# Performance work log

Measured on AMD Instinct MI355X. Metric: run time of the kernel, lower is better.

## Reference

```python
import jax, jax.numpy as jnp
import numpy as np
from jax import lax

IN_C, OUT_C, K, Z_DIM, GROUPS = 256, 256, 3, 64, 1
B, H, W = 16, 32, 32


def setup_inputs() -> dict:
    key = jax.random.key(0)
    k1, k2, k3 = jax.random.split(key, 3)
    x = jax.random.normal(k1, (B, IN_C, H, W), dtype=jnp.float32)
    z = jax.random.normal(k2, (B, Z_DIM), dtype=jnp.float32)
    # nn.Linear(z_dim, groups*out_per_group*in_per_group*k*k, bias=False).weight
    fan = GROUPS * (OUT_C // GROUPS) * (IN_C // GROUPS) * K * K  # 589824
    w_lin = jax.random.normal(k3, (fan, Z_DIM), dtype=jnp.float32) * (1.0 / np.sqrt(Z_DIM))
    return {"x": x, "z": z, "w_lin": w_lin}


def reference(x, z, w_lin):
    b = x.shape[0]
    in_per_group = IN_C // GROUPS
    # hypernetwork: per-sample conv weights [B, out_c, in_c/groups, k, k]
    Wgen = (z @ w_lin.T).reshape(b, OUT_C, in_per_group, K, K)
    pad = K // 2

    def conv_one(xi, Wi):
        # xi: [in_c, H, W], Wi: [out_c, in_c/groups, k, k]
        y = lax.conv_general_dilated(
            xi[None], Wi,
            window_strides=(1, 1),
            padding=[(pad, pad), (pad, pad)],
            dimension_numbers=("NCHW", "OIHW", "NCHW"),
            feature_group_count=GROUPS,
        )
        return y[0]

    return jax.vmap(conv_one)(x, Wgen)  # [B, out_c, H, W]
```

## Files before the change

### kernel.cpp

```cpp
#include <hip/hip_runtime.h>

#define PB_ 589824
#define XT_PB 295936
#define XGR 544

typedef __bf16 bf16;
typedef __bf16 bf16x4 __attribute__((ext_vector_type(4)));
typedef __bf16 bf16x8 __attribute__((ext_vector_type(8)));
typedef float f32x4 __attribute__((ext_vector_type(4)));

static __device__ inline bf16x8 cvt8(float4 a, float4 b) {
  bf16x8 r;
  r[0] = (bf16)a.x; r[1] = (bf16)a.y; r[2] = (bf16)a.z; r[3] = (bf16)a.w;
  r[4] = (bf16)b.x; r[5] = (bf16)b.y; r[6] = (bf16)b.z; r[7] = (bf16)b.w;
  return r;
}

__global__ __launch_bounds__(256) void prep_kernel(const float* __restrict__ z,
                                                   const float* __restrict__ wl,
                                                   const float* __restrict__ x,
                                                   bf16* __restrict__ WgA,
                                                   bf16* __restrict__ xt) {
  const int bid = blockIdx.x;
  if (bid < 1152) {
    __shared__ __align__(16) char wsm[16384];
    const int c_  = bid & 7;
    const int tap = (bid >> 3) % 9;
    const int ob  = bid / 72;
    const int lane = threadIdx.x & 63;
    const int wave = threadIdx.x >> 6;
    const int l15 = lane & 15;
    const int q = lane >> 4;

    const float* zp = z + l15 * 64 + q * 8;
    bf16x8 bz[2];
#pragma unroll
    for (int kc = 0; kc < 2; ++kc)
      bz[kc] = cvt8(*(const float4*)(zp + kc * 32), *(const float4*)(zp + kc * 32 + 4));

#pragma unroll
    for (int mi = 0; mi < 4; ++mi) {
      const int m = wave * 4 + mi;
#pragma unroll
      for (int h = 0; h < 2; ++h) {
        const long t = (long)(ob * 16 + m) * 2304 + (c_ * 32 + h * 16 + l15) * 9 + tap;
        const float* wp = wl + t * 64 + q * 8;
        f32x4 acc = {0.f, 0.f, 0.f, 0.f};
#pragma unroll
        for (int kc = 0; kc < 2; ++kc) {
          bf16x8 aw = cvt8(*(const float4*)(wp + kc * 32), *(const float4*)(wp + kc * 32 + 4));
          acc = __builtin_amdgcn_mfma_f32_16x16x32_bf16(aw, bz[kc], acc, 0, 0, 0);
        }
        bf16x4 o;
        o[0] = (bf16)acc[0]; o[1] = (bf16)acc[1]; o[2] = (bf16)acc[2]; o[3] = (bf16)acc[3];
        const int elem = ((h * 2 + (q >> 1)) * 16 + m) * 8 + (q & 1) * 4;
        int byte = (l15 << 10) + elem * 2;
        byte ^= (l15 & 7) << 4;
        *(bf16x4*)(wsm + byte) = o;
      }
    }
    __syncthreads();
    const int b = threadIdx.x >> 4;
    const int l16 = threadIdx.x & 15;
    const long gbase = ((((long)b * 16 + ob) * 9 + tap) * 8 + c_) * 512;
#pragma unroll
    for (int i = 0; i < 4; ++i) {
      int byte = (b << 10) + (l16 << 4) + (i << 8);
      byte ^= (b & 7) << 4;
      uint4 v = *(const uint4*)(wsm + byte);
      *(uint4*)(WgA + gbase + l16 * 8 + i * 128) = v;
    }
  } else if (bid < 1416) {
    int g = (bid - 1152) * 256 + threadIdx.x;
    int b = g / 4224;
    int rem = g - b * 4224;
    int pi = rem >> 5;
    int gq = rem & 31;
    int p;
    if (pi < 34) p = pi;
    else if (pi < 68) p = 1122 + (pi - 34);
    else {
      int k = (pi - 68) >> 1;
      p = (k + 1) * 34 + (((pi - 68) & 1) ? 33 : 0);
    }
    *(uint4*)(xt + (long)b * XT_PB + p * 256 + gq * 8) = make_uint4(0u, 0u, 0u, 0u);
  } else {
    __shared__ bf16 tile[32][33];
    int i = bid - 1416;
    int row = i & 31, c0 = ((i >> 5) & 7) * 32, b = i >> 8;
    int l = threadIdx.x & 31;
    int r = threadIdx.x >> 5;
#pragma unroll
    for (int j = 0; j < 4; ++j) {
      int ch = r + j * 8;
      tile[ch][l] = (bf16)x[((b * 256 + c0 + ch) * 1024) + row * 32 + l];
    }
    __syncthreads();
#pragma unroll
    for (int j = 0; j < 4; ++j) {
      int col = r + j * 8;
      xt[(long)b * XT_PB + ((row + 1) * 34 + (col + 1)) * 256 + c0 + l] = tile[l][col];
    }
  }
}

__global__ __launch_bounds__(256, 4) void conv_kernel(const bf16* __restrict__ WgA,
                                                      const bf16* __restrict__ xt,
                                                      float* __restrict__ y) {
  __shared__ __align__(16) bf16 xs[2][XGR * 8];
  const int id = blockIdx.x;
  const int xcd = id & 7;
  const int k = id >> 3;
  const int b = ((k & 1) << 3) | xcd;
  const int r2 = k >> 1;
  const int mt = r2 & 3;
  const int nt = r2 >> 2;
  const int tid = threadIdx.x;
  const int lane = tid & 63;
  const int wave = tid >> 6;
  const int wm = wave & 1;
  const int wn = wave >> 1;
  const int l15 = lane & 15;
  const int q = lane >> 4;
  const int oc0 = mt * 64;

  const bf16* xtb = xt + (long)b * XT_PB;
  const bf16* xstage = xtb + (nt * 2) * 34 * 256;
  const bf16* Wb = WgA + (long)b * PB_;
  const bf16* Wlane = Wb + (long)((oc0 >> 4) + wm * 2) * 9 * 8 * 512 + lane * 8;

  f32x4 acc[2][2] = {};
  bf16x8 afr[2][3][2];

#define LOADA(KH, C, SLOT)                                                       \
  {                                                                              \
    _Pragma("unroll")                                                            \
    for (int kw_ = 0; kw_ < 3; ++kw_)                                            \
      _Pragma("unroll")                                                          \
      for (int mi_ = 0; mi_ < 2; ++mi_)                                          \
        afr[SLOT][kw_][mi_] = *(const bf16x8*)(                                  \
            Wlane + (long)(((mi_ * 9 + (KH) * 3 + kw_) * 8 + (C)) * 512));       \
  }

#define STAGE(IC0, SEL)                                                          \
  for (int g0 = wave * 64; g0 < XGR; g0 += 256) {                                \
    int g = g0 + lane;                                                           \
    int pix = g >> 2, slot = g & 3;                                              \
    int qq = slot ^ ((pix >> 1) & 3);                                            \
    if (g < XGR) {                                                               \
      const bf16* src = xstage + (pix * 256 + (IC0) + qq * 8);                   \
      __builtin_amdgcn_global_load_lds(                                          \
          (const __attribute__((address_space(1))) void*)src,                    \
          (__attribute__((address_space(3))) void*)(&xs[SEL][g0 * 8]), 16, 0, 0);\
    }                                                                            \
  }

#define ROW(KH, SLOT, BUF, PF)                                                   \
  {                                                                              \
    PF                                                                           \
    _Pragma("unroll")                                                            \
    for (int kw = 0; kw < 3; ++kw) {                                             \
      bf16x8 bfr[2];                                                             \
      _Pragma("unroll")                                                          \
      for (int n = 0; n < 2; ++n) {                                              \
        int pl = wn * 32 + n * 16;                                               \
        int pr = pl >> 5;                                                        \
        int pc = (pl & 31) + l15;                                                \
        int spix = (pr + (KH)) * 34 + pc + kw;                                   \
        bfr[n] = *(const bf16x8*)((BUF) + spix * 32 +                            \
                                  ((((spix >> 1) & 3) ^ q) * 8));                \
      }                                                                          \
      _Pragma("unroll")                                                          \
      for (int mi = 0; mi < 2; ++mi)                                             \
        _Pragma("unroll")                                                        \
        for (int n = 0; n < 2; ++n)                                              \
          acc[mi][n] = __builtin_amdgcn_mfma_f32_16x16x32_bf16(                  \
              afr[SLOT][kw][mi], bfr[n], acc[mi][n], 0, 0, 0);                   \
    }                                                                            \
  }

  STAGE(0, 0)
  LOADA(0, 0, 0)
  for (int c2 = 0; c2 < 4; ++c2) {
    const int ce = c2 * 2;
    {
      __syncthreads();
      STAGE((ce + 1) * 32, (ce + 1) & 1)
      const bf16* buf = &xs[ce & 1][0];
      ROW(0, 0, buf, LOADA(1, ce, 1))
      ROW(1, 1, buf, LOADA(2, ce, 0))
      ROW(2, 0, buf, LOADA(0, ce + 1, 1))
    }
    {
      const int co = ce + 1;
      __syncthreads();
      if (co < 7) { STAGE((co + 1) * 32, (co + 1) & 1) }
      const bf16* buf = &xs[co & 1][0];
      ROW(0, 1, buf, LOADA(1, co, 0))
      ROW(1, 0, buf, LOADA(2, co, 1))
      if (co < 7) { ROW(2, 1, buf, LOADA(0, co + 1, 0)) }
      else        { ROW(2, 1, buf, ) }
    }
  }

#pragma unroll
  for (int mi = 0; mi < 2; ++mi) {
    int ocb = oc0 + (wm * 2 + mi) * 16 + q * 4;
#pragma unroll
    for (int n = 0; n < 2; ++n) {
      int p = nt * 64 + wn * 32 + n * 16 + l15;
      float* yp = y + ((long)b * 256 + ocb) * 1024 + p;
#pragma unroll
      for (int rr = 0; rr < 4; ++rr)
        yp[rr * 1024] = acc[mi][n][rr];
    }
  }
#undef STAGE
#undef LOADA
#undef ROW
}

extern "C" void kernel_launch(void* const* d_in, const int* in_sizes, int n_in,
                              void* d_out, int out_size, void* d_ws, size_t ws_size,
                              hipStream_t stream) {
  const float* x  = (const float*)d_in[0];
  const float* z  = (const float*)d_in[1];
  const float* wl = (const float*)d_in[2];
  float* y = (float*)d_out;
  bf16* WgA = (bf16*)d_ws;
  bf16* xt  = (bf16*)((char*)d_ws + 18874368);

  prep_kernel<<<5512, 256, 0, stream>>>(z, wl, x, WgA, xt);
  conv_kernel<<<1024, 256, 0, stream>>>(WgA, xt, y);
}
```

Baseline: 269.5 us.

## Give each conv block a 4-row pixel tile and each wave 16 channels by 128 pixels

Each block now covers 128 output pixels (4 image rows) instead of 64, so the grid is halved to 512 blocks and launch bounds drop to 2 blocks per CU. Each wave computes 16 output channels across all 128 pixels instead of a 32x32 tile. This halves redundant global-to-LDS staging of the input halo and the per-wave weight-fragment loads. In exchange, the kernel does one LDS B-fragment read per MFMA instead of one per two MFMAs, and has fewer blocks to hide latency with.

```diff
diff --git a/kernel.cpp b/kernel.cpp
--- a/kernel.cpp
+++ b/kernel.cpp
@@ -2,7 +2,7 @@
 
 #define PB_ 589824
 #define XT_PB 295936
-#define XGR 544
+#define XGR2 816
 
 typedef __bf16 bf16;
 typedef __bf16 bf16x4 __attribute__((ext_vector_type(4)));
@@ -104,10 +104,10 @@
   }
 }
 
-__global__ __launch_bounds__(256, 4) void conv_kernel(const bf16* __restrict__ WgA,
+__global__ __launch_bounds__(256, 2) void conv_kernel(const bf16* __restrict__ WgA,
                                                       const bf16* __restrict__ xt,
                                                       float* __restrict__ y) {
-  __shared__ __align__(16) bf16 xs[2][XGR * 8];
+  __shared__ __align__(16) bf16 xs[2][XGR2 * 8];
   const int id = blockIdx.x;
   const int xcd = id & 7;
   const int k = id >> 3;
@@ -118,36 +118,32 @@
   const int tid = threadIdx.x;
   const int lane = tid & 63;
   const int wave = tid >> 6;
-  const int wm = wave & 1;
-  const int wn = wave >> 1;
   const int l15 = lane & 15;
   const int q = lane >> 4;
-  const int oc0 = mt * 64;
 
   const bf16* xtb = xt + (long)b * XT_PB;
-  const bf16* xstage = xtb + (nt * 2) * 34 * 256;
+  const bf16* xstage = xtb + (nt * 4) * 34 * 256;
   const bf16* Wb = WgA + (long)b * PB_;
-  const bf16* Wlane = Wb + (long)((oc0 >> 4) + wm * 2) * 9 * 8 * 512 + lane * 8;
-
-  f32x4 acc[2][2] = {};
-  bf16x8 afr[2][3][2];
+  const int ob = mt * 4 + wave;
+  const bf16* Wlane = Wb + (long)ob * 9 * 8 * 512 + lane * 8;
+
+  f32x4 acc[8] = {};
+  bf16x8 afr[2][3];
 
 #define LOADA(KH, C, SLOT)                                                       \
   {                                                                              \
     _Pragma("unroll")                                                            \
     for (int kw_ = 0; kw_ < 3; ++kw_)                                            \
-      _Pragma("unroll")                                                          \
-      for (int mi_ = 0; mi_ < 2; ++mi_)                                          \
-        afr[SLOT][kw_][mi_] = *(const bf16x8*)(                                  \
-            Wlane + (long)(((mi_ * 9 + (KH) * 3 + kw_) * 8 + (C)) * 512));       \
+      afr[SLOT][kw_] = *(const bf16x8*)(                                         \
+          Wlane + (long)((((KH) * 3 + kw_) * 8 + (C)) * 512));                   \
   }
 
 #define STAGE(IC0, SEL)                                                          \
-  for (int g0 = wave * 64; g0 < XGR; g0 += 256) {                                \
+  for (int g0 = wave * 64; g0 < XGR2; g0 += 256) {                               \
     int g = g0 + lane;                                                           \
     int pix = g >> 2, slot = g & 3;                                              \
     int qq = slot ^ ((pix >> 1) & 3);                                            \
-    if (g < XGR) {                                                               \
+    if (g < XGR2) {                                                              \
       const bf16* src = xstage + (pix * 256 + (IC0) + qq * 8);                   \
       __builtin_amdgcn_global_load_lds(                                          \
           (const __attribute__((address_space(1))) void*)src,                    \
@@ -160,22 +156,17 @@
     PF                                                                           \
     _Pragma("unroll")                                                            \
     for (int kw = 0; kw < 3; ++kw) {                                             \
-      bf16x8 bfr[2];                                                             \
       _Pragma("unroll")                                                          \
-      for (int n = 0; n < 2; ++n) {                                              \
-        int pl = wn * 32 + n * 16;                                               \
+      for (int n = 0; n < 8; ++n) {                                              \
+        int pl = n * 16;                                                         \
         int pr = pl >> 5;                                                        \
         int pc = (pl & 31) + l15;                                                \
-        int spix = (pr + (KH)) * 34 + pc + kw;                                   \
-        bfr[n] = *(const bf16x8*)((BUF) + spix * 32 +                            \
-                                  ((((spix >> 1) & 3) ^ q) * 8));                \
+        int spix = (pr + (KH)) * 34 + pc + kw;                       \
+        bf16x8 bfr = *(const bf16x8*)((BUF) + spix * 32 +                        \
+                                      ((((spix >> 1) & 3) ^ q) * 8));            \
+        acc[n] = __builtin_amdgcn_mfma_f32_16x16x32_bf16(                        \
+            afr[SLOT][kw], bfr, acc[n], 0, 0, 0);                                \
       }                                                                          \
-      _Pragma("unroll")                                                          \
-      for (int mi = 0; mi < 2; ++mi)                                             \
-        _Pragma("unroll")                                                        \
-        for (int n = 0; n < 2; ++n)                                              \
-          acc[mi][n] = __builtin_amdgcn_mfma_f32_16x16x32_bf16(                  \
-              afr[SLOT][kw][mi], bfr[n], acc[mi][n], 0, 0, 0);                   \
     }                                                                            \
   }
 
@@ -203,16 +194,15 @@
     }
   }
 
-#pragma unroll
-  for (int mi = 0; mi < 2; ++mi) {
-    int ocb = oc0 + (wm * 2 + mi) * 16 + q * 4;
-#pragma unroll
-    for (int n = 0; n < 2; ++n) {
-      int p = nt * 64 + wn * 32 + n * 16 + l15;
+  {
+    const int ocb = mt * 64 + wave * 16 + q * 4;
+#pragma unroll
+    for (int n = 0; n < 8; ++n) {
+      int p = nt * 128 + n * 16 + l15;
       float* yp = y + ((long)b * 256 + ocb) * 1024 + p;
 #pragma unroll
       for (int rr = 0; rr < 4; ++rr)
-        yp[rr * 1024] = acc[mi][n][rr];
+        yp[rr * 1024] = acc[n][rr];
     }
   }
 #undef STAGE
@@ -231,5 +221,5 @@
   bf16* xt  = (bf16*)((char*)d_ws + 18874368);
 
   prep_kernel<<<5512, 256, 0, stream>>>(z, wl, x, WgA, xt);
-  conv_kernel<<<1024, 256, 0, stream>>>(WgA, xt, y);
-}
+  conv_kernel<<<512, 256, 0, stream>>>(WgA, xt, y);
+}
```

After: 256.0 us. 5.0% less time.
